# Optimization experiments

Hardware: AMD Instinct MI355X
Metric: run time of the kernel (lower is better)

The kernel has to match this reference:

```python
import jax, jax.numpy as jnp
import numpy as np

TOP_K = 8
N_EXPERTS = 64
HIDDEN = 4096


def setup_inputs() -> dict:
    key = jax.random.key(0)
    k1, k2 = jax.random.split(key)
    hidden_states = jax.random.normal(k1, (4, 4096, HIDDEN), dtype=jnp.float32)
    # kaiming_uniform_(a=sqrt(5)) on a (64, 4096) weight -> U(-b, b), b = sqrt(6/((1+5)*4096)) = 1/sqrt(4096)
    bound = 1.0 / np.sqrt(HIDDEN)
    weight = jax.random.uniform(k2, (N_EXPERTS, HIDDEN), dtype=jnp.float32,
                                minval=-bound, maxval=bound)
    return {"hidden_states": hidden_states, "weight": weight}


def reference(hidden_states, weight):
    bsz, seq_len, h = hidden_states.shape
    x = hidden_states.reshape(-1, h)                       # [T, H]
    logits = jnp.einsum('th,eh->te', x, weight)            # [T, E]
    scores = jax.nn.softmax(logits, axis=-1)
    topk_weight, topk_idx = jax.lax.top_k(scores, TOP_K)   # [T, K]
    denom = jnp.sum(topk_weight, axis=-1, keepdims=True) + 1e-20
    topk_weight = topk_weight / denom
    topk_weight = topk_weight.reshape(bsz, seq_len, TOP_K)
    topk_idx = topk_idx.reshape(bsz, seq_len, TOP_K)
    # training-time aux loss (seq_aux path): histogram of argmax expert * mean prob
    probs = scores                                         # softmax(logits)
    top1 = jnp.argmax(probs, axis=-1)                      # [T]
    counts = jnp.zeros((N_EXPERTS,), dtype=jnp.float32).at[top1].add(1.0)
    route_prob = jnp.mean(probs, axis=0)                   # [E]
    route_frac = counts / jnp.sum(counts)
    aux_loss = jnp.sum(route_prob * route_frac) * N_EXPERTS
    return topk_idx, topk_weight, aux_loss
```

## Files before the change

### kernel.cpp

```cpp
#include <hip/hip_runtime.h>
#include <hip/hip_bf16.h>

#define TOKS 16384
#define HID  4096
#define NEXP 64
#define EPS  1e-4f

#define WS_FLAGCNT  128
#define WS_FLAGLIST 192
#define WS_BPACK    16576

typedef __attribute__((ext_vector_type(8))) short short8_t;
typedef __attribute__((ext_vector_type(4))) float f32x4;

static __device__ __forceinline__ unsigned short f2bf_rn(float x) {
    unsigned u = __builtin_bit_cast(unsigned, x);
    u = (u + 0x7fffu + ((u >> 16) & 1u)) >> 16;
    return (unsigned short)u;
}
static __device__ __forceinline__ float bf2f(unsigned short h) {
    return __builtin_bit_cast(float, (unsigned)h << 16);
}
static __device__ __forceinline__ void gl2lds16(const void* g, void* l) {
    __builtin_amdgcn_global_load_lds(
        (const __attribute__((address_space(1))) unsigned int*)g,
        (__attribute__((address_space(3))) unsigned int*)l, 16, 0, 0);
}

__global__ void moe_prep(const float* __restrict__ W, unsigned short* __restrict__ Bpk,
                         float* __restrict__ wsf) {
    const int idx = blockIdx.x * blockDim.x + threadIdx.x;
    if (idx < 192) wsf[idx] = 0.0f;
    if (idx >= NEXP * HID) return;
    const int n = idx >> 12;
    const int k = idx & 4095;
    const float w = W[idx];
    const unsigned short hi = f2bf_rn(w);
    const unsigned short lo = f2bf_rn(w - bf2f(hi));
    const int kt   = k >> 5;
    const int nt   = n >> 4;
    const int lane = (n & 15) | (((k >> 3) & 3) << 4);
    const int j    = k & 7;
    const int dst  = (((kt << 2) + nt) << 10) + (lane << 3) + j;
    Bpk[dst]       = hi;
    Bpk[dst + 512] = lo;
}

__global__ __launch_bounds__(512, 2)
void moe_fused(const float* __restrict__ X, const unsigned short* __restrict__ Bpk,
               float* __restrict__ out, float* __restrict__ wsf) {
    __shared__ __align__(16) float xbuf[2][64][64];
    __shared__ __align__(16) unsigned short bbuf[2][8192];
    float (*L)[68] = (float (*)[68])&xbuf[0][0][0];

    const int tid  = threadIdx.x;
    const int lane = tid & 63;
    const int w    = tid >> 6;
    const int mt   = w & 3;
    const int nh   = w >> 2;
    const int g    = lane >> 4;
    const int tok0 = blockIdx.x * 64;

    f32x4 acc[2];
    acc[0] = (f32x4){0.f, 0.f, 0.f, 0.f};
    acc[1] = (f32x4){0.f, 0.f, 0.f, 0.f};

    #define STAGE(buf, s)                                                            \
    {                                                                                \
        const int k0_ = (s) << 6;                                                    \
        _Pragma("unroll")                                                            \
        for (int i = 0; i < 2; ++i) {                                                \
            const int rg = (w << 3) + (i << 2) + g;                                  \
            const int ck = (lane & 15) ^ (rg & 15);                                  \
            gl2lds16(X + (size_t)(tok0 + rg) * HID + k0_ + (ck << 2),                \
                     (void*)&xbuf[buf][(w << 3) + (i << 2)][0]);                     \
        }                                                                            \
        _Pragma("unroll")                                                            \
        for (int j = 0; j < 2; ++j) {                                                \
            const int c1k = (w << 1) + j;                                            \
            gl2lds16((const char*)Bpk + ((size_t)(s) << 14) + (c1k << 10) + (lane << 4), \
                     (void*)((char*)&bbuf[buf][0] + (c1k << 10)));                   \
        }                                                                            \
    }

    STAGE(0, 0);
    __syncthreads();

    const int tr = (mt << 4) + (lane & 15);
    const char* arow = (const char*)&xbuf[0][tr][0];
    const int rsw = lane & 15;

    for (int s = 0; s < 64; ++s) {
        const int cur = s & 1;
        if (s < 63) STAGE(cur ^ 1, s + 1);

        const char* ab = arow + cur * 16384;
        const char* bb = (const char*)&bbuf[cur][0];
        #pragma unroll
        for (int ktl = 0; ktl < 2; ++ktl) {
            const int cl = (ktl << 3) + (g << 1);
            const float4 a0 = *(const float4*)(ab + ((cl ^ rsw) << 4));
            const float4 a1 = *(const float4*)(ab + (((cl + 1) ^ rsw) << 4));
            const float xv[8] = {a0.x, a0.y, a0.z, a0.w, a1.x, a1.y, a1.z, a1.w};
            short8_t ah, al;
            #pragma unroll
            for (int j = 0; j < 8; ++j) {
                const unsigned short h = f2bf_rn(xv[j]);
                ah[j] = (short)h;
                al[j] = (short)f2bf_rn(xv[j] - bf2f(h));
            }
            #pragma unroll
            for (int ntl = 0; ntl < 2; ++ntl) {
                const char* bp = bb + (((ktl << 2) + (nh << 1) + ntl) << 11) + (lane << 4);
                const short8_t bh = *(const short8_t*)bp;
                const short8_t bl = *(const short8_t*)(bp + 1024);
                acc[ntl] = __builtin_amdgcn_mfma_f32_16x16x32_bf16(ah, bh, acc[ntl], 0, 0, 0);
                acc[ntl] = __builtin_amdgcn_mfma_f32_16x16x32_bf16(al, bh, acc[ntl], 0, 0, 0);
                acc[ntl] = __builtin_amdgcn_mfma_f32_16x16x32_bf16(ah, bl, acc[ntl], 0, 0, 0);
            }
        }
        __syncthreads();
    }

    #pragma unroll
    for (int ntl = 0; ntl < 2; ++ntl)
        #pragma unroll
        for (int r = 0; r < 4; ++r)
            L[(mt << 4) + (g << 2) + r][(nh << 5) + (ntl << 4) + (lane & 15)] = acc[ntl][r];
    __syncthreads();

    float* outIdx = out;
    float* outW   = out + TOKS * 8;
    int* flagcnt  = (int*)wsf + WS_FLAGCNT;
    int* flaglist = (int*)wsf + WS_FLAGLIST;

    float rp = 0.f;
    #pragma unroll
    for (int tt = 0; tt < 8; ++tt) {
        const int tl = (w << 3) + tt;
        const float lg = L[tl][lane];

        float v = lg; int idx = lane;
        #pragma unroll
        for (int size = 2; size <= 64; size <<= 1) {
            #pragma unroll
            for (int str = size >> 1; str > 0; str >>= 1) {
                const float ov = __shfl_xor(v, str, 64);
                const int   oi = __shfl_xor(idx, str, 64);
                const bool pb = (ov > v) || (ov == v && oi < idx);
                const bool keepFirst = ((lane & str) == 0) == ((lane & size) == 0);
                if (pb == keepFirst) { v = ov; idx = oi; }
            }
        }

        const float m = __shfl(v, 0, 64);
        const float p = __expf(lg - m);
        float sdenom = p;
        #pragma unroll
        for (int o = 32; o; o >>= 1) sdenom += __shfl_xor(sdenom, o, 64);
        const float inv_s = 1.0f / sdenom;
        rp += p * inv_s;

        const float wkv = __expf(v - m) * inv_s;
        float d8 = (lane < 8) ? wkv : 0.f;
        #pragma unroll
        for (int o = 1; o < 8; o <<= 1) d8 += __shfl_xor(d8, o, 64);
        const float invd = 1.0f / (d8 + 1e-20f);
        const float nv = __shfl_down(v, 1, 64);
        const bool flg = __any(lane < 8 && (v - nv) < EPS);

        const int gtok = tok0 + tl;
        if (lane < 8) {
            outIdx[(size_t)gtok * 8 + lane] = (float)idx;
            outW[(size_t)gtok * 8 + lane]   = wkv * invd;
        }
        if (lane == 0) {
            atomicAdd(&wsf[NEXP + idx], 1.0f);
            if (flg) {
                const int pos = atomicAdd(flagcnt, 1);
                if (pos < TOKS) flaglist[pos] = gtok;
            }
        }
    }
    atomicAdd(&wsf[lane], rp);
    #undef STAGE
}

__global__ __launch_bounds__(256, 2)
void moe_fix(const float* __restrict__ X, const float* __restrict__ W,
             float* __restrict__ out, float* __restrict__ wsf) {
    __shared__ double red[256];
    const int tid = threadIdx.x;
    const int e   = tid & 63;
    const int kc  = tid >> 6;
    const int nf  = min(*((int*)wsf + WS_FLAGCNT), TOKS);
    const int* flaglist = (const int*)wsf + WS_FLAGLIST;
    float* outIdx = out;
    float* outW   = out + TOKS * 8;

    for (int fi = blockIdx.x; fi < nf; fi += gridDim.x) {
        const int tok = flaglist[fi];
        const float* xrow = X + (size_t)tok * HID + kc * 1024;
        const float* wrow = W + (size_t)e  * HID + kc * 1024;
        double part = 0.0;
        for (int j = 0; j < 1024; j += 4) {
            const float4 xv = *(const float4*)(xrow + j);
            const float4 wv = *(const float4*)(wrow + j);
            part = fma((double)xv.x, (double)wv.x, part);
            part = fma((double)xv.y, (double)wv.y, part);
            part = fma((double)xv.z, (double)wv.z, part);
            part = fma((double)xv.w, (double)wv.w, part);
        }
        red[tid] = part;
        __syncthreads();
        if (tid < 64) {
            const double lg = ((red[tid] + red[64 + tid]) + red[128 + tid]) + red[192 + tid];
            const float lgf = (float)lg;
            float m = lgf;
            #pragma unroll
            for (int o = 32; o; o >>= 1) m = fmaxf(m, __shfl_xor(m, o, 64));
            const float p = __expf(lgf - m);
            float s = p;
            #pragma unroll
            for (int o = 32; o; o >>= 1) s += __shfl_xor(s, o, 64);
            const float inv_s = 1.0f / s;

            double v = lg;
            double bw[8]; int ik[8];
            #pragma unroll
            for (int k = 0; k < 8; ++k) {
                double bv = v; int bi = tid;
                #pragma unroll
                for (int o = 32; o; o >>= 1) {
                    const double ov = __shfl_xor(bv, o, 64);
                    const int    oi = __shfl_xor(bi, o, 64);
                    if (ov > bv || (ov == bv && oi < bi)) { bv = ov; bi = oi; }
                }
                bw[k] = bv; ik[k] = bi;
                if (tid == bi) v = -1.0e300;
            }
            float wk[8]; float denom = 1e-20f;
            #pragma unroll
            for (int k = 0; k < 8; ++k) {
                wk[k] = __expf((float)bw[k] - m) * inv_s; denom += wk[k];
            }
            const float invd = 1.0f / denom;
            const size_t base = (size_t)tok * 8;
            const int oldtop = (int)outIdx[base];
            if (tid < 8) {
                outIdx[base + tid] = (float)ik[tid];
                outW[base + tid]   = wk[tid] * invd;
            }
            if (tid == 0 && ik[0] != oldtop) {
                atomicAdd(&wsf[NEXP + oldtop], -1.0f);
                atomicAdd(&wsf[NEXP + ik[0]],  1.0f);
            }
        }
        __syncthreads();
    }
}

__global__ void moe_final(const float* __restrict__ wsf, float* __restrict__ out) {
    const int e = threadIdx.x;
    float v = wsf[e] * wsf[NEXP + e];
    #pragma unroll
    for (int o = 32; o; o >>= 1) v += __shfl_xor(v, o, 64);
    if (e == 0)
        out[2 * TOKS * 8] = v * (64.0f / ((float)TOKS * (float)TOKS));
}

__global__ void moe_init(float* __restrict__ wsf, int n) {
    const int i = blockIdx.x * blockDim.x + threadIdx.x;
    if (i < n) wsf[i] = 0.0f;
}

__global__ void moe_w_cvt(const float* __restrict__ W, double* __restrict__ Wd) {
    const int i = blockIdx.x * blockDim.x + threadIdx.x;
    if (i < NEXP * HID) Wd[i] = (double)W[i];
}

__global__ __launch_bounds__(512, 2)
void moe_mono(const float* __restrict__ X, const double* __restrict__ Wd,
              float* __restrict__ out, float* __restrict__ wsf) {
    __shared__ double xs[64][66];
    __shared__ double L2[64][65];
    const int tid  = threadIdx.x;
    const int lane = tid & 63;
    const int wid  = __builtin_amdgcn_readfirstlane(tid >> 6);
    const int tok0 = blockIdx.x * 64;
    double acc[8] = {0., 0., 0., 0., 0., 0., 0., 0.};
    for (int h0 = 0; h0 < HID; h0 += 64) {
        #pragma unroll
        for (int i = 0; i < 8; ++i) {
            const int li = tid + i * 512;
            xs[li >> 6][li & 63] = (double)X[((size_t)(tok0 + (li >> 6)) << 12) + (h0 + (li & 63))];
        }
        __syncthreads();
        const double* wchunk = Wd + (((size_t)(wid << 3)) << 12) + h0;
        #pragma unroll 2
        for (int hh = 0; hh < 64; hh += 2) {
            const double2 xv = *(const double2*)&xs[lane][hh];
            #pragma unroll
            for (int e = 0; e < 8; ++e) {
                const double* wr = wchunk + (((size_t)e) << 12) + hh;
                acc[e] = fma(xv.x, wr[0], acc[e]);
                acc[e] = fma(xv.y, wr[1], acc[e]);
            }
        }
        __syncthreads();
    }
    #pragma unroll
    for (int e = 0; e < 8; ++e) L2[lane][(wid << 3) + e] = acc[e];
    __syncthreads();
    float* outIdx = out;
    float* outW   = out + (TOKS * 8);
    float rp = 0.0f;
    for (int tt = 0; tt < 8; ++tt) {
        const int t = (wid << 3) + tt;
        const double lg = L2[t][lane];
        const float lgf = (float)lg;
        float m = lgf;
        #pragma unroll
        for (int o = 32; o; o >>= 1) m = fmaxf(m, __shfl_xor(m, o, 64));
        const float p = __expf(lgf - m);
        float s = p;
        #pragma unroll
        for (int o = 32; o; o >>= 1) s += __shfl_xor(s, o, 64);
        const float inv_s = 1.0f / s;
        rp += p * inv_s;
        double v = lg;
        float wk[8]; int ik[8];
        #pragma unroll
        for (int k = 0; k < 8; ++k) {
            double bv = v; int bi = lane;
            #pragma unroll
            for (int o = 32; o; o >>= 1) {
                const double ov = __shfl_xor(bv, o, 64);
                const int    oi = __shfl_xor(bi, o, 64);
                if (ov > bv || (ov == bv && oi < bi)) { bv = ov; bi = oi; }
            }
            wk[k] = __expf((float)bv - m) * inv_s; ik[k] = bi;
            if (lane == bi) v = -1.0e300;
        }
        if (lane == 0) {
            const float denom = (((wk[0]+wk[1])+(wk[2]+wk[3])) +
                                 ((wk[4]+wk[5])+(wk[6]+wk[7]))) + 1e-20f;
            const float invd = 1.0f / denom;
            const size_t base = ((size_t)(tok0 + t)) << 3;
            #pragma unroll
            for (int k = 0; k < 8; ++k) {
                outIdx[base + k] = (float)ik[k];
                outW[base + k]   = wk[k] * invd;
            }
            atomicAdd(&wsf[NEXP + ik[0]], 1.0f);
        }
    }
    atomicAdd(&wsf[lane], rp);
}

extern "C" void kernel_launch(void* const* d_in, const int* in_sizes, int n_in,
                              void* d_out, int out_size, void* d_ws, size_t ws_size,
                              hipStream_t stream) {
    const float* X = (const float*)d_in[0];
    const float* W = (const float*)d_in[1];
    float* out = (float*)d_out;
    float* wsf = (float*)d_ws;

    const size_t need = 4ull * WS_BPACK + 2ull * 524288;

    if (ws_size >= need) {
        unsigned short* Bpk = (unsigned short*)(wsf + WS_BPACK);
        moe_prep<<<(NEXP * HID + 255) / 256, 256, 0, stream>>>(W, Bpk, wsf);
        moe_fused<<<TOKS / 64, 512, 0, stream>>>(X, Bpk, out, wsf);
        moe_fix<<<256, 256, 0, stream>>>(X, W, out, wsf);
        moe_final<<<1, 64, 0, stream>>>(wsf, out);
    } else {
        double* Wd = (double*)d_ws;
        float* wsf2 = (float*)(Wd + NEXP * HID);
        moe_w_cvt<<<(NEXP * HID + 255) / 256, 256, 0, stream>>>(W, Wd);
        moe_init<<<1, 256, 0, stream>>>(wsf2, 128);
        moe_mono<<<TOKS / 64, 512, 0, stream>>>(X, Wd, out, wsf2);
        moe_final<<<1, 64, 0, stream>>>(wsf2, out);
    }
}
```

Baseline: 236.8 us.

## Deepen staging to four LDS buffers with prefetch distance two and truncated bf16 split

Expands the LDS ring from two to four buffers and prefetches two K-stages ahead. Each iteration now ends with a partial vmcnt wait plus one barrier instead of a full __syncthreads, so global loads overlap more of the MFMA work. Separately, the hi/lo bf16 split of X now uses truncation instead of round-to-nearest, which cuts ALU work in the inner loop. The cost is doubled shared memory, which drops occupancy to one block per CU. The truncated split also changes rounding slightly, though hi+lo still approximates the fp32 value closely.

```diff
diff --git a/kernel.cpp b/kernel.cpp
--- a/kernel.cpp
+++ b/kernel.cpp
@@ -46,11 +46,11 @@
     Bpk[dst + 512] = lo;
 }
 
-__global__ __launch_bounds__(512, 2)
+__global__ __launch_bounds__(512, 1)
 void moe_fused(const float* __restrict__ X, const unsigned short* __restrict__ Bpk,
                float* __restrict__ out, float* __restrict__ wsf) {
-    __shared__ __align__(16) float xbuf[2][64][64];
-    __shared__ __align__(16) unsigned short bbuf[2][8192];
+    __shared__ __align__(16) float xbuf[4][64][64];
+    __shared__ __align__(16) unsigned short bbuf[4][8192];
     float (*L)[68] = (float (*)[68])&xbuf[0][0][0];
 
     const int tid  = threadIdx.x;
@@ -65,36 +65,41 @@
     acc[0] = (f32x4){0.f, 0.f, 0.f, 0.f};
     acc[1] = (f32x4){0.f, 0.f, 0.f, 0.f};
 
-    #define STAGE(buf, s)                                                            \
-    {                                                                                \
-        const int k0_ = (s) << 6;                                                    \
-        _Pragma("unroll")                                                            \
-        for (int i = 0; i < 2; ++i) {                                                \
-            const int rg = (w << 3) + (i << 2) + g;                                  \
-            const int ck = (lane & 15) ^ (rg & 15);                                  \
-            gl2lds16(X + (size_t)(tok0 + rg) * HID + k0_ + (ck << 2),                \
-                     (void*)&xbuf[buf][(w << 3) + (i << 2)][0]);                     \
-        }                                                                            \
-        _Pragma("unroll")                                                            \
-        for (int j = 0; j < 2; ++j) {                                                \
-            const int c1k = (w << 1) + j;                                            \
-            gl2lds16((const char*)Bpk + ((size_t)(s) << 14) + (c1k << 10) + (lane << 4), \
-                     (void*)((char*)&bbuf[buf][0] + (c1k << 10)));                   \
-        }                                                                            \
+    #define STAGE(bf, ss)                                                              \
+    {                                                                                  \
+        const int k0_ = (ss) << 6;                                                     \
+        _Pragma("unroll")                                                              \
+        for (int i = 0; i < 2; ++i) {                                                  \
+            const int rg = (w << 3) + (i << 2) + g;                                    \
+            const int ck = (lane & 15) ^ (rg & 15);                                    \
+            gl2lds16(X + (size_t)(tok0 + rg) * HID + k0_ + (ck << 2),                  \
+                     (void*)&xbuf[bf][(w << 3) + (i << 2)][0]);                        \
+        }                                                                              \
+        _Pragma("unroll")                                                              \
+        for (int j = 0; j < 2; ++j) {                                                  \
+            const int c1k = (w << 1) + j;                                              \
+            gl2lds16((const char*)Bpk + ((size_t)(ss) << 14) + (c1k << 10) + (lane << 4), \
+                     (void*)((char*)&bbuf[bf][0] + (c1k << 10)));                      \
+        }                                                                              \
     }
 
     STAGE(0, 0);
-    __syncthreads();
-
-    const int tr = (mt << 4) + (lane & 15);
-    const char* arow = (const char*)&xbuf[0][tr][0];
+    STAGE(1, 1);
+
+    const int tr  = (mt << 4) + (lane & 15);
     const int rsw = lane & 15;
 
     for (int s = 0; s < 64; ++s) {
-        const int cur = s & 1;
-        if (s < 63) STAGE(cur ^ 1, s + 1);
-
-        const char* ab = arow + cur * 16384;
+        const int cur = s & 3;
+        {
+            const int ss = (s + 2 < 64) ? (s + 2) : 63;
+            STAGE((s + 2) & 3, ss);
+        }
+        asm volatile("s_waitcnt vmcnt(8)" ::: "memory");
+        __builtin_amdgcn_s_barrier();
+        __builtin_amdgcn_sched_barrier(0);
+
+        const char* ab = (const char*)&xbuf[cur][tr][0];
         const char* bb = (const char*)&bbuf[cur][0];
         #pragma unroll
         for (int ktl = 0; ktl < 2; ++ktl) {
@@ -105,9 +110,10 @@
             short8_t ah, al;
             #pragma unroll
             for (int j = 0; j < 8; ++j) {
-                const unsigned short h = f2bf_rn(xv[j]);
-                ah[j] = (short)h;
-                al[j] = (short)f2bf_rn(xv[j] - bf2f(h));
+                const unsigned u = __builtin_bit_cast(unsigned, xv[j]);
+                ah[j] = (short)(u >> 16);
+                const float hif = __builtin_bit_cast(float, u & 0xFFFF0000u);
+                al[j] = (short)(__builtin_bit_cast(unsigned, xv[j] - hif) >> 16);
             }
             #pragma unroll
             for (int ntl = 0; ntl < 2; ++ntl) {
@@ -119,8 +125,9 @@
                 acc[ntl] = __builtin_amdgcn_mfma_f32_16x16x32_bf16(ah, bl, acc[ntl], 0, 0, 0);
             }
         }
-        __syncthreads();
-    }
+    }
+    asm volatile("s_waitcnt vmcnt(0)" ::: "memory");
+    __syncthreads();
 
     #pragma unroll
     for (int ntl = 0; ntl < 2; ++ntl)
```

After: 212.1 us. -10.4%, faster.
